# Performance work log

Measured on AMD Instinct MI355X. Metric: run time of the kernel, lower is better.

The kernel has to match this reference:

```python
import jax, jax.numpy as jnp
import numpy as np


def setup_inputs() -> dict:
    key = jax.random.key(0)
    k1, k2 = jax.random.split(key)
    B, A, H, W, C = 4, 9, 256, 256, 9
    F = 64
    lfi = jax.random.normal(k1, (B, A, H, W, C), dtype=jnp.float32)
    f_maps = jax.random.uniform(k2, (B, H, W, F), dtype=jnp.float32)
    return {"lfi": lfi, "f_maps": f_maps}


def reference(lfi, f_maps):
    # height mask: per (b, filter), mean of the [h,w] map over rows, normalized by its max.
    # f_maps: [B, H, W, F] -> hv: [B, W, F]; note original asserts W == H.
    hv = jnp.mean(f_maps, axis=1)                      # [B, W, F]
    hv = hv / jnp.max(hv, axis=1, keepdims=True)       # normalize per (b, f)
    h_mask = jnp.transpose(hv, (0, 2, 1))              # [B, F, H]
    # lfi: [B, A, H, W, C]; h_feat[b,f] = lfi[b] * h_mask[b,f,:] broadcast over H axis,
    # then mean over angular dims A and C -> factorizes as mean(lfi) * h_mask.
    m = jnp.mean(lfi, axis=(1, 4))                     # [B, H, W]
    out = jnp.einsum('bhw,bfh->bhwf', m, h_mask)       # [B, H, W, F]
    return out
```

## Files before the change

### kernel.cpp

```cpp
#include <hip/hip_runtime.h>

#define BB 4
#define AA 9
#define HH 256
#define WW 256
#define CC 9
#define FF 64

__global__ __launch_bounds__(256) void k_stage1(const float* __restrict__ fm,
                                                const float* __restrict__ lfi,
                                                float* __restrict__ hv,
                                                int* __restrict__ maxbuf,
                                                float* __restrict__ m) {
    if (blockIdx.x < BB * WW) {
        const int blk = blockIdx.x;
        const int b = blk >> 8;
        const int w = blk & 255;
        const int f4 = threadIdx.x & 15;
        const int hl = threadIdx.x >> 4;

        const float4* base =
            (const float4*)fm + (((size_t)b * HH) * WW + w) * (FF / 4) + f4;
        float4 acc = make_float4(0.f, 0.f, 0.f, 0.f);
#pragma unroll
        for (int h = hl; h < HH; h += 16) {
            float4 v = base[(size_t)h * WW * (FF / 4)];
            acc.x += v.x; acc.y += v.y; acc.z += v.z; acc.w += v.w;
        }
        __shared__ float sm[16 * FF];
        ((float4*)sm)[hl * 16 + f4] = acc;
        __syncthreads();
        if (threadIdx.x < FF) {
            const int f = threadIdx.x;
            float t = 0.f;
#pragma unroll
            for (int j = 0; j < 16; ++j) t += sm[j * FF + f];
            t *= (1.0f / HH);
            hv[(size_t)blk * FF + f] = t;
            atomicMax(maxbuf + b * FF + f, __float_as_int(t));
        }
    } else {
        const int gid = (blockIdx.x - BB * WW) * 256 + threadIdx.x;
        const int b = gid >> 16;
        const int hw = gid & 65535;

        const size_t astride = (size_t)HH * WW * CC;
        const float* base = lfi + (size_t)b * AA * astride + (size_t)hw * CC;

        float s = 0.f;
#pragma unroll
        for (int a = 0; a < AA; ++a) {
            const float* p = base + (size_t)a * astride;
#pragma unroll
            for (int c = 0; c < CC; ++c) s += p[c];
        }
        m[gid] = s * (1.0f / (AA * CC));
    }
}

__global__ __launch_bounds__(256) void k_out(const float* __restrict__ m,
                                             const float* __restrict__ hv,
                                             const int* __restrict__ maxbuf,
                                             float4* __restrict__ out) {
    const int idx = blockIdx.x * 256 + threadIdx.x;
    const int f4 = idx & 15;
    const int rest = idx >> 4;
    const int h = (rest >> 8) & 255;
    const int b = rest >> 16;

    const float mv = m[rest];
    const float4 hv4 = ((const float4*)hv)[((size_t)(b * HH + h)) * (FF / 4) + f4];
    const int4 mx4 = ((const int4*)maxbuf)[b * (FF / 4) + f4];

    float4 o;
    o.x = mv * hv4.x / __int_as_float(mx4.x);
    o.y = mv * hv4.y / __int_as_float(mx4.y);
    o.z = mv * hv4.z / __int_as_float(mx4.z);
    o.w = mv * hv4.w / __int_as_float(mx4.w);
    out[idx] = o;
}

extern "C" void kernel_launch(void* const* d_in, const int* in_sizes, int n_in,
                              void* d_out, int out_size, void* d_ws, size_t ws_size,
                              hipStream_t stream) {
    const float* lfi = (const float*)d_in[0];
    const float* fm  = (const float*)d_in[1];
    float* out = (float*)d_out;

    char* ws = (char*)d_ws;
    float* hv  = (float*)ws;
    int*   mxb = (int*)(ws + (size_t)BB * WW * FF * 4);
    float* m   = (float*)(ws + (size_t)BB * WW * FF * 4 + 1024);

    hipMemsetAsync(mxb, 0, BB * FF * sizeof(int), stream);
    k_stage1<<<BB * WW + (BB * HH * WW) / 256, 256, 0, stream>>>(fm, lfi, hv, mxb, m);
    k_out<<<(BB * HH * WW * FF / 4) / 256, 256, 0, stream>>>(m, hv, mxb, (float4*)out);
}
```

Before: 47.83 us.

## Restructure f_maps column reduction into row-chunk partials plus separate reduce kernel

The f_maps mean over H is now computed by blocks that each stream a contiguous chunk of full rows, using coalesced float4 loads and 16 accumulators per thread. Each block writes a partial-sum plane, and a new reduce kernel sums the partials, writes hv and does a per-block max before the atomicMax. This replaces the old per-(b,w) strided column walk. The lfi mean path now stages each angular slice through LDS with coalesced float4 loads instead of strided per-thread scalar reads. The cost is an extra kernel launch and partial-buffer traffic, and the chunk count is chosen from the workspace size.

```diff
diff --git a/kernel.cpp b/kernel.cpp
--- a/kernel.cpp
+++ b/kernel.cpp
@@ -6,55 +6,94 @@
 #define WW 256
 #define CC 9
 #define FF 64
+#define WF (WW * FF)
+#define WF4 (WF / 4)
 
-__global__ __launch_bounds__(256) void k_stage1(const float* __restrict__ fm,
-                                                const float* __restrict__ lfi,
-                                                float* __restrict__ hv,
-                                                int* __restrict__ maxbuf,
-                                                float* __restrict__ m) {
-    if (blockIdx.x < BB * WW) {
-        const int blk = blockIdx.x;
-        const int b = blk >> 8;
-        const int w = blk & 255;
-        const int f4 = threadIdx.x & 15;
-        const int hl = threadIdx.x >> 4;
+template <int NCH>
+__global__ __launch_bounds__(256, 2) void k_stage1(const float* __restrict__ fm,
+                                                   const float* __restrict__ lfi,
+                                                   float* __restrict__ partial,
+                                                   float* __restrict__ m) {
+    constexpr int R = HH / NCH;
+    const int t = threadIdx.x;
 
-        const float4* base =
-            (const float4*)fm + (((size_t)b * HH) * WW + w) * (FF / 4) + f4;
-        float4 acc = make_float4(0.f, 0.f, 0.f, 0.f);
+    if (blockIdx.x < BB * NCH) {
+        const int b = blockIdx.x / NCH;
+        const int ch = blockIdx.x % NCH;
+        const float4* row = (const float4*)fm + (size_t)(b * HH + ch * R) * WF4;
+
+        float4 acc[16];
 #pragma unroll
-        for (int h = hl; h < HH; h += 16) {
-            float4 v = base[(size_t)h * WW * (FF / 4)];
-            acc.x += v.x; acc.y += v.y; acc.z += v.z; acc.w += v.w;
+        for (int k = 0; k < 16; ++k) acc[k] = make_float4(0.f, 0.f, 0.f, 0.f);
+
+        for (int r = 0; r < R; ++r) {
+#pragma unroll
+            for (int k = 0; k < 16; ++k) {
+                float4 v = row[(size_t)r * WF4 + k * 256 + t];
+                acc[k].x += v.x; acc[k].y += v.y; acc[k].z += v.z; acc[k].w += v.w;
+            }
         }
-        __shared__ float sm[16 * FF];
-        ((float4*)sm)[hl * 16 + f4] = acc;
-        __syncthreads();
-        if (threadIdx.x < FF) {
-            const int f = threadIdx.x;
-            float t = 0.f;
+        float4* pout = (float4*)partial + (size_t)(b * NCH + ch) * WF4;
 #pragma unroll
-            for (int j = 0; j < 16; ++j) t += sm[j * FF + f];
-            t *= (1.0f / HH);
-            hv[(size_t)blk * FF + f] = t;
-            atomicMax(maxbuf + b * FF + f, __float_as_int(t));
-        }
+        for (int k = 0; k < 16; ++k) pout[k * 256 + t] = acc[k];
     } else {
-        const int gid = (blockIdx.x - BB * WW) * 256 + threadIdx.x;
-        const int b = gid >> 16;
-        const int hw = gid & 65535;
+        const int blkm = blockIdx.x - BB * NCH;
+        const int b = blkm >> 8;
+        const int hw0 = (blkm & 255) * 256;
 
+        __shared__ float lds[256 * CC];
         const size_t astride = (size_t)HH * WW * CC;
-        const float* base = lfi + (size_t)b * AA * astride + (size_t)hw * CC;
+        const float* base = lfi + (size_t)b * AA * astride + (size_t)hw0 * CC;
 
         float s = 0.f;
+        for (int a = 0; a < AA; ++a) {
+            const float4* src = (const float4*)(base + (size_t)a * astride);
+            float4* l4 = (float4*)lds;
+            l4[t] = src[t];
+            l4[t + 256] = src[t + 256];
+            if (t < 64) l4[t + 512] = src[t + 512];
+            __syncthreads();
+            float ps = 0.f;
 #pragma unroll
-        for (int a = 0; a < AA; ++a) {
-            const float* p = base + (size_t)a * astride;
+            for (int c = 0; c < CC; ++c) ps += lds[t * CC + c];
+            s += ps;
+            __syncthreads();
+        }
+        m[(size_t)blkm * 256 + t] = s * (1.0f / (AA * CC));
+    }
+}
+
+template <int NCH>
+__global__ __launch_bounds__(256) void k_reduce(const float* __restrict__ partial,
+                                                float* __restrict__ hv,
+                                                int* __restrict__ maxbuf) {
+    const int t = threadIdx.x;
+    const int b = blockIdx.x >> 4;
+    const int i = blockIdx.x & 15;
+    const int wf4 = i * 256 + t;
+
+    const float4* p4 = (const float4*)partial + (size_t)b * NCH * WF4 + wf4;
+    float4 s = make_float4(0.f, 0.f, 0.f, 0.f);
 #pragma unroll
-            for (int c = 0; c < CC; ++c) s += p[c];
-        }
-        m[gid] = s * (1.0f / (AA * CC));
+    for (int ch = 0; ch < NCH; ++ch) {
+        float4 v = p4[(size_t)ch * WF4];
+        s.x += v.x; s.y += v.y; s.z += v.z; s.w += v.w;
+    }
+    s.x *= (1.0f / HH); s.y *= (1.0f / HH); s.z *= (1.0f / HH); s.w *= (1.0f / HH);
+    ((float4*)hv)[(size_t)b * WF4 + wf4] = s;
+
+    __shared__ float lmax[16][FF];
+    const int wl = t >> 4, f4 = t & 15;
+    lmax[wl][f4 * 4 + 0] = s.x;
+    lmax[wl][f4 * 4 + 1] = s.y;
+    lmax[wl][f4 * 4 + 2] = s.z;
+    lmax[wl][f4 * 4 + 3] = s.w;
+    __syncthreads();
+    if (t < FF) {
+        float mx = lmax[0][t];
+#pragma unroll
+        for (int j = 1; j < 16; ++j) mx = fmaxf(mx, lmax[j][t]);
+        atomicMax(maxbuf + b * FF + t, __float_as_int(mx));
     }
 }
 
@@ -69,7 +108,7 @@
     const int b = rest >> 16;
 
     const float mv = m[rest];
-    const float4 hv4 = ((const float4*)hv)[((size_t)(b * HH + h)) * (FF / 4) + f4];
+    const float4 hv4 = ((const float4*)hv)[(size_t)(b * HH + h) * (FF / 4) + f4];
     const int4 mx4 = ((const int4*)maxbuf)[b * (FF / 4) + f4];
 
     float4 o;
@@ -80,19 +119,38 @@
     out[idx] = o;
 }
 
+template <int NCH>
+static void run_pipeline(const float* lfi, const float* fm, float* out,
+                         char* ws, hipStream_t stream) {
+    float* hv = (float*)ws;
+    int* mxb = (int*)(ws + (size_t)BB * WW * FF * 4);
+    float* m = (float*)(ws + (size_t)BB * WW * FF * 4 + 4096);
+    float* partial = (float*)(ws + (size_t)BB * WW * FF * 4 + 4096 +
+                              (size_t)BB * HH * WW * 4);
+
+    hipMemsetAsync(mxb, 0, BB * FF * sizeof(int), stream);
+    k_stage1<NCH><<<BB * NCH + 1024, 256, 0, stream>>>(fm, lfi, partial, m);
+    k_reduce<NCH><<<BB * 16, 256, 0, stream>>>(partial, hv, mxb);
+    k_out<<<(BB * HH * WW * FF / 4) / 256, 256, 0, stream>>>(m, hv, mxb,
+                                                             (float4*)out);
+}
+
 extern "C" void kernel_launch(void* const* d_in, const int* in_sizes, int n_in,
                               void* d_out, int out_size, void* d_ws, size_t ws_size,
                               hipStream_t stream) {
     const float* lfi = (const float*)d_in[0];
     const float* fm  = (const float*)d_in[1];
     float* out = (float*)d_out;
+    char* ws = (char*)d_ws;
 
-    char* ws = (char*)d_ws;
-    float* hv  = (float*)ws;
-    int*   mxb = (int*)(ws + (size_t)BB * WW * FF * 4);
-    float* m   = (float*)(ws + (size_t)BB * WW * FF * 4 + 1024);
+    const size_t head = (size_t)BB * WW * FF * 4 + 4096 + (size_t)BB * HH * WW * 4;
+    const size_t plane = (size_t)BB * WF * 4;
 
-    hipMemsetAsync(mxb, 0, BB * FF * sizeof(int), stream);
-    k_stage1<<<BB * WW + (BB * HH * WW) / 256, 256, 0, stream>>>(fm, lfi, hv, mxb, m);
-    k_out<<<(BB * HH * WW * FF / 4) / 256, 256, 0, stream>>>(m, hv, mxb, (float4*)out);
+    if (ws_size >= head + 64 * plane) {
+        run_pipeline<64>(lfi, fm, out, ws, stream);
+    } else if (ws_size >= head + 32 * plane) {
+        run_pipeline<32>(lfi, fm, out, ws, stream);
+    } else {
+        run_pipeline<16>(lfi, fm, out, ws, stream);
+    }
 }
```

New measurement: 55.69 us. +16.4%, slower.

## Split height reduction into partial sums and vectorize lfi angular reduction

Applied to the files above, without the earlier changes.

The column-mean reduction over f_maps now runs as a separate kernel. Each block sums a slice of rows for 16 columns into partial buffers, and a second pass combines the partials, writes hv and does a block-local max before one atomicMax per filter. The lfi mean now has each thread handle four pixels with float4 loads, with the angular dimension split across two roles whose partial sums k_out adds together. The output kernel replaces the division with a hardware reciprocal. This adds an extra kernel launch and workspace traffic, and the reciprocal may differ slightly from exact division.

```diff
diff --git a/kernel.cpp b/kernel.cpp
--- a/kernel.cpp
+++ b/kernel.cpp
@@ -6,61 +6,93 @@
 #define WW 256
 #define CC 9
 #define FF 64
+#define WF (WW * FF)
+#define WF4 (WF / 4)
+#define NHQ 8
+#define HQR (HH / NHQ)
 
-__global__ __launch_bounds__(256) void k_stage1(const float* __restrict__ fm,
-                                                const float* __restrict__ lfi,
-                                                float* __restrict__ hv,
-                                                int* __restrict__ maxbuf,
-                                                float* __restrict__ m) {
-    if (blockIdx.x < BB * WW) {
-        const int blk = blockIdx.x;
-        const int b = blk >> 8;
-        const int w = blk & 255;
-        const int f4 = threadIdx.x & 15;
-        const int hl = threadIdx.x >> 4;
+__global__ __launch_bounds__(256) void k_hv(const float* __restrict__ fm,
+                                            float* __restrict__ partial) {
+    const int t = threadIdx.x;
+    const int wc = blockIdx.x & 15;
+    const int hq = (blockIdx.x >> 4) & (NHQ - 1);
+    const int b = blockIdx.x >> 7;
+
+    const float* base = fm + ((size_t)(b * HH + hq * HQR) * WW + wc * 16) * FF +
+                        (t >> 4) * FF + (t & 15) * 4;
+    float4 acc = make_float4(0.f, 0.f, 0.f, 0.f);
+#pragma unroll 8
+    for (int h = 0; h < HQR; ++h) {
+        float4 v = *(const float4*)(base + (size_t)h * WW * FF);
+        acc.x += v.x; acc.y += v.y; acc.z += v.z; acc.w += v.w;
+    }
+    ((float4*)partial)[(size_t)(b * NHQ + hq) * WF4 + wc * 256 + t] = acc;
+}
+
+__global__ __launch_bounds__(256) void k_mred(const float* __restrict__ lfi,
+                                              const float* __restrict__ partial,
+                                              float* __restrict__ mpart,
+                                              float* __restrict__ hv,
+                                              int* __restrict__ mxb) {
+    const int t = threadIdx.x;
+    if (blockIdx.x < 512) {
+        const int role = blockIdx.x >> 8;
+        const int hw4 = (blockIdx.x & 255) * 256 + t;
+        const int b = hw4 >> 14;
+        const int hwl = (hw4 & 16383) * 4;
+        const size_t astride = (size_t)HH * WW * CC;
+        const int a0 = role ? 5 : 0;
+        const int a1 = role ? 9 : 5;
 
         const float4* base =
-            (const float4*)fm + (((size_t)b * HH) * WW + w) * (FF / 4) + f4;
+            (const float4*)(lfi + (size_t)b * AA * astride + (size_t)hwl * CC);
         float4 acc = make_float4(0.f, 0.f, 0.f, 0.f);
+        for (int a = a0; a < a1; ++a) {
+            const float4* p = base + (size_t)a * (astride / 4);
+            float4 v0 = p[0], v1 = p[1], v2 = p[2], v3 = p[3], v4 = p[4];
+            float4 v5 = p[5], v6 = p[6], v7 = p[7], v8 = p[8];
+            acc.x += v0.x + v0.y + v0.z + v0.w + v1.x + v1.y + v1.z + v1.w + v2.x;
+            acc.y += v2.y + v2.z + v2.w + v3.x + v3.y + v3.z + v3.w + v4.x + v4.y;
+            acc.z += v4.z + v4.w + v5.x + v5.y + v5.z + v5.w + v6.x + v6.y + v6.z;
+            acc.w += v6.w + v7.x + v7.y + v7.z + v7.w + v8.x + v8.y + v8.z + v8.w;
+        }
+        ((float4*)mpart)[(size_t)role * 65536 + hw4] = acc;
+    } else {
+        const int rb = blockIdx.x - 512;
+        const int b = rb >> 4;
+        const int i = rb & 15;
+        const int wf4 = i * 256 + t;
+
+        const float4* p4 = (const float4*)partial + (size_t)b * NHQ * WF4 + wf4;
+        float4 s = make_float4(0.f, 0.f, 0.f, 0.f);
 #pragma unroll
-        for (int h = hl; h < HH; h += 16) {
-            float4 v = base[(size_t)h * WW * (FF / 4)];
-            acc.x += v.x; acc.y += v.y; acc.z += v.z; acc.w += v.w;
+        for (int hq = 0; hq < NHQ; ++hq) {
+            float4 v = p4[(size_t)hq * WF4];
+            s.x += v.x; s.y += v.y; s.z += v.z; s.w += v.w;
         }
-        __shared__ float sm[16 * FF];
-        ((float4*)sm)[hl * 16 + f4] = acc;
+        s.x *= (1.0f / HH); s.y *= (1.0f / HH);
+        s.z *= (1.0f / HH); s.w *= (1.0f / HH);
+        ((float4*)hv)[(size_t)b * WF4 + wf4] = s;
+
+        __shared__ float lmax[16][FF];
+        const int wl = t >> 4, f4 = t & 15;
+        lmax[wl][f4 * 4 + 0] = s.x;
+        lmax[wl][f4 * 4 + 1] = s.y;
+        lmax[wl][f4 * 4 + 2] = s.z;
+        lmax[wl][f4 * 4 + 3] = s.w;
         __syncthreads();
-        if (threadIdx.x < FF) {
-            const int f = threadIdx.x;
-            float t = 0.f;
+        if (t < FF) {
+            float mx = lmax[0][t];
 #pragma unroll
-            for (int j = 0; j < 16; ++j) t += sm[j * FF + f];
-            t *= (1.0f / HH);
-            hv[(size_t)blk * FF + f] = t;
-            atomicMax(maxbuf + b * FF + f, __float_as_int(t));
+            for (int j = 1; j < 16; ++j) mx = fmaxf(mx, lmax[j][t]);
+            atomicMax(mxb + b * FF + t, __float_as_int(mx));
         }
-    } else {
-        const int gid = (blockIdx.x - BB * WW) * 256 + threadIdx.x;
-        const int b = gid >> 16;
-        const int hw = gid & 65535;
-
-        const size_t astride = (size_t)HH * WW * CC;
-        const float* base = lfi + (size_t)b * AA * astride + (size_t)hw * CC;
-
-        float s = 0.f;
-#pragma unroll
-        for (int a = 0; a < AA; ++a) {
-            const float* p = base + (size_t)a * astride;
-#pragma unroll
-            for (int c = 0; c < CC; ++c) s += p[c];
-        }
-        m[gid] = s * (1.0f / (AA * CC));
     }
 }
 
-__global__ __launch_bounds__(256) void k_out(const float* __restrict__ m,
+__global__ __launch_bounds__(256) void k_out(const float* __restrict__ mpart,
                                              const float* __restrict__ hv,
-                                             const int* __restrict__ maxbuf,
+                                             const int* __restrict__ mxb,
                                              float4* __restrict__ out) {
     const int idx = blockIdx.x * 256 + threadIdx.x;
     const int f4 = idx & 15;
@@ -68,15 +100,16 @@
     const int h = (rest >> 8) & 255;
     const int b = rest >> 16;
 
-    const float mv = m[rest];
-    const float4 hv4 = ((const float4*)hv)[((size_t)(b * HH + h)) * (FF / 4) + f4];
-    const int4 mx4 = ((const int4*)maxbuf)[b * (FF / 4) + f4];
+    const float mv =
+        (mpart[rest] + mpart[262144 + rest]) * (1.0f / (AA * CC));
+    const float4 hv4 = ((const float4*)hv)[(size_t)(b * HH + h) * (FF / 4) + f4];
+    const int4 mx4 = ((const int4*)mxb)[b * (FF / 4) + f4];
 
     float4 o;
-    o.x = mv * hv4.x / __int_as_float(mx4.x);
-    o.y = mv * hv4.y / __int_as_float(mx4.y);
-    o.z = mv * hv4.z / __int_as_float(mx4.z);
-    o.w = mv * hv4.w / __int_as_float(mx4.w);
+    o.x = mv * hv4.x * __builtin_amdgcn_rcpf(__int_as_float(mx4.x));
+    o.y = mv * hv4.y * __builtin_amdgcn_rcpf(__int_as_float(mx4.y));
+    o.z = mv * hv4.z * __builtin_amdgcn_rcpf(__int_as_float(mx4.z));
+    o.w = mv * hv4.w * __builtin_amdgcn_rcpf(__int_as_float(mx4.w));
     out[idx] = o;
 }
 
@@ -86,13 +119,16 @@
     const float* lfi = (const float*)d_in[0];
     const float* fm  = (const float*)d_in[1];
     float* out = (float*)d_out;
+    char* ws = (char*)d_ws;
 
-    char* ws = (char*)d_ws;
-    float* hv  = (float*)ws;
-    int*   mxb = (int*)(ws + (size_t)BB * WW * FF * 4);
-    float* m   = (float*)(ws + (size_t)BB * WW * FF * 4 + 1024);
+    float* hv = (float*)ws;
+    int* mxb = (int*)(ws + 262144);
+    float* mpart = (float*)(ws + 262144 + 4096);
+    float* partial = (float*)(ws + 262144 + 4096 + 2097152);
 
     hipMemsetAsync(mxb, 0, BB * FF * sizeof(int), stream);
-    k_stage1<<<BB * WW + (BB * HH * WW) / 256, 256, 0, stream>>>(fm, lfi, hv, mxb, m);
-    k_out<<<(BB * HH * WW * FF / 4) / 256, 256, 0, stream>>>(m, hv, mxb, (float4*)out);
+    k_hv<<<BB * NHQ * 16, 256, 0, stream>>>(fm, partial);
+    k_mred<<<512 + BB * 16, 256, 0, stream>>>(lfi, partial, mpart, hv, mxb);
+    k_out<<<(BB * HH * WW * FF / 4) / 256, 256, 0, stream>>>(mpart, hv, mxb,
+                                                             (float4*)out);
 }
```

New measurement: 49.44 us. 3.4% more time.

## Fuse lfi angular mean into output kernel and split hv reduction kernel

Applied to the files above, without the earlier changes.

Moves the lfi mean computation out of the first kernel and into the output kernel. Each block computes m for one (b,h) row into LDS and then writes all 64 filter outputs for that row, so the m intermediate no longer goes to global memory. The hv reduction now uses a two-level shared-memory tree and issues four atomics per thread. Division is replaced by a hardware reciprocal applied once per thread. The trade-off is less overlap between the lfi reads and the f_maps reduction, plus slightly lower precision from the approximate reciprocal.

```diff
diff --git a/kernel.cpp b/kernel.cpp
--- a/kernel.cpp
+++ b/kernel.cpp
@@ -7,77 +7,97 @@
 #define CC 9
 #define FF 64
 
-__global__ __launch_bounds__(256) void k_stage1(const float* __restrict__ fm,
-                                                const float* __restrict__ lfi,
-                                                float* __restrict__ hv,
-                                                int* __restrict__ maxbuf,
-                                                float* __restrict__ m) {
-    if (blockIdx.x < BB * WW) {
-        const int blk = blockIdx.x;
-        const int b = blk >> 8;
-        const int w = blk & 255;
-        const int f4 = threadIdx.x & 15;
-        const int hl = threadIdx.x >> 4;
+__global__ __launch_bounds__(256) void k_hv(const float* __restrict__ fm,
+                                            float* __restrict__ hv,
+                                            int* __restrict__ mxb) {
+    const int t = threadIdx.x;
+    const int w = blockIdx.x & 255;
+    const int b = blockIdx.x >> 8;
+    const int f4 = t & 15;
+    const int hl = t >> 4;
 
-        const float4* base =
-            (const float4*)fm + (((size_t)b * HH) * WW + w) * (FF / 4) + f4;
-        float4 acc = make_float4(0.f, 0.f, 0.f, 0.f);
+    const float4* base = (const float4*)fm +
+                         ((size_t)(b * HH + hl) * WW + w) * (FF / 4) + f4;
+    const size_t hstep = (size_t)16 * WW * (FF / 4);
+    float4 acc = make_float4(0.f, 0.f, 0.f, 0.f);
 #pragma unroll
-        for (int h = hl; h < HH; h += 16) {
-            float4 v = base[(size_t)h * WW * (FF / 4)];
-            acc.x += v.x; acc.y += v.y; acc.z += v.z; acc.w += v.w;
-        }
-        __shared__ float sm[16 * FF];
-        ((float4*)sm)[hl * 16 + f4] = acc;
-        __syncthreads();
-        if (threadIdx.x < FF) {
-            const int f = threadIdx.x;
-            float t = 0.f;
-#pragma unroll
-            for (int j = 0; j < 16; ++j) t += sm[j * FF + f];
-            t *= (1.0f / HH);
-            hv[(size_t)blk * FF + f] = t;
-            atomicMax(maxbuf + b * FF + f, __float_as_int(t));
-        }
-    } else {
-        const int gid = (blockIdx.x - BB * WW) * 256 + threadIdx.x;
-        const int b = gid >> 16;
-        const int hw = gid & 65535;
+    for (int i = 0; i < 16; ++i) {
+        float4 v = base[i * hstep];
+        acc.x += v.x; acc.y += v.y; acc.z += v.z; acc.w += v.w;
+    }
 
-        const size_t astride = (size_t)HH * WW * CC;
-        const float* base = lfi + (size_t)b * AA * astride + (size_t)hw * CC;
-
-        float s = 0.f;
-#pragma unroll
-        for (int a = 0; a < AA; ++a) {
-            const float* p = base + (size_t)a * astride;
-#pragma unroll
-            for (int c = 0; c < CC; ++c) s += p[c];
-        }
-        m[gid] = s * (1.0f / (AA * CC));
+    __shared__ float4 sm[16][16];
+    __shared__ float4 sm2[4][16];
+    sm[hl][f4] = acc;
+    __syncthreads();
+    if (t < 64) {
+        const int q = t >> 4, f = t & 15;
+        float4 s0 = sm[q * 4 + 0][f], s1 = sm[q * 4 + 1][f];
+        float4 s2 = sm[q * 4 + 2][f], s3 = sm[q * 4 + 3][f];
+        float4 r;
+        r.x = (s0.x + s1.x) + (s2.x + s3.x);
+        r.y = (s0.y + s1.y) + (s2.y + s3.y);
+        r.z = (s0.z + s1.z) + (s2.z + s3.z);
+        r.w = (s0.w + s1.w) + (s2.w + s3.w);
+        sm2[q][f] = r;
+    }
+    __syncthreads();
+    if (t < 16) {
+        float4 s0 = sm2[0][t], s1 = sm2[1][t], s2 = sm2[2][t], s3 = sm2[3][t];
+        float4 r;
+        r.x = ((s0.x + s1.x) + (s2.x + s3.x)) * (1.0f / HH);
+        r.y = ((s0.y + s1.y) + (s2.y + s3.y)) * (1.0f / HH);
+        r.z = ((s0.z + s1.z) + (s2.z + s3.z)) * (1.0f / HH);
+        r.w = ((s0.w + s1.w) + (s2.w + s3.w)) * (1.0f / HH);
+        ((float4*)hv)[(size_t)(b * WW + w) * (FF / 4) + t] = r;
+        int* mp = mxb + b * FF + t * 4;
+        atomicMax(mp + 0, __float_as_int(r.x));
+        atomicMax(mp + 1, __float_as_int(r.y));
+        atomicMax(mp + 2, __float_as_int(r.z));
+        atomicMax(mp + 3, __float_as_int(r.w));
     }
 }
 
-__global__ __launch_bounds__(256) void k_out(const float* __restrict__ m,
-                                             const float* __restrict__ hv,
-                                             const int* __restrict__ maxbuf,
-                                             float4* __restrict__ out) {
-    const int idx = blockIdx.x * 256 + threadIdx.x;
-    const int f4 = idx & 15;
-    const int rest = idx >> 4;
-    const int h = (rest >> 8) & 255;
-    const int b = rest >> 16;
+__global__ __launch_bounds__(256) void k_mout(const float* __restrict__ lfi,
+                                              const float* __restrict__ hv,
+                                              const int* __restrict__ mxb,
+                                              float4* __restrict__ out) {
+    const int t = threadIdx.x;
+    const int bh = blockIdx.x;
+    const int b = bh >> 8;
+    const int h = bh & 255;
+    const int f4 = t & 15;
 
-    const float mv = m[rest];
-    const float4 hv4 = ((const float4*)hv)[((size_t)(b * HH + h)) * (FF / 4) + f4];
-    const int4 mx4 = ((const int4*)maxbuf)[b * (FF / 4) + f4];
+    const float4 hv4 = ((const float4*)hv)[(size_t)bh * (FF / 4) + f4];
+    const int4 mx4 = ((const int4*)mxb)[b * (FF / 4) + f4];
+    float4 hvn;
+    hvn.x = hv4.x * __builtin_amdgcn_rcpf(__int_as_float(mx4.x));
+    hvn.y = hv4.y * __builtin_amdgcn_rcpf(__int_as_float(mx4.y));
+    hvn.z = hv4.z * __builtin_amdgcn_rcpf(__int_as_float(mx4.z));
+    hvn.w = hv4.w * __builtin_amdgcn_rcpf(__int_as_float(mx4.w));
 
-    float4 o;
-    o.x = mv * hv4.x / __int_as_float(mx4.x);
-    o.y = mv * hv4.y / __int_as_float(mx4.y);
-    o.z = mv * hv4.z / __int_as_float(mx4.z);
-    o.w = mv * hv4.w / __int_as_float(mx4.w);
-    out[idx] = o;
+    const size_t astride = (size_t)HH * WW * CC;
+    const float* base = lfi + (size_t)b * AA * astride +
+                        ((size_t)h * WW + t) * CC;
+    float s = 0.f;
+#pragma unroll
+    for (int a = 0; a < AA; ++a) {
+        const float* p = base + (size_t)a * astride;
+#pragma unroll
+        for (int c = 0; c < CC; ++c) s += p[c];
+    }
+    __shared__ float m_lds[WW];
+    m_lds[t] = s * (1.0f / (AA * CC));
+    __syncthreads();
+
+    float4* ob = out + (size_t)bh * (WW * FF / 4);
+#pragma unroll
+    for (int k = 0; k < 16; ++k) {
+        const float mv = m_lds[k * 16 + (t >> 4)];
+        float4 o;
+        o.x = mv * hvn.x; o.y = mv * hvn.y; o.z = mv * hvn.z; o.w = mv * hvn.w;
+        ob[k * 256 + t] = o;
+    }
 }
 
 extern "C" void kernel_launch(void* const* d_in, const int* in_sizes, int n_in,
@@ -86,13 +106,12 @@
     const float* lfi = (const float*)d_in[0];
     const float* fm  = (const float*)d_in[1];
     float* out = (float*)d_out;
+    char* ws = (char*)d_ws;
 
-    char* ws = (char*)d_ws;
-    float* hv  = (float*)ws;
-    int*   mxb = (int*)(ws + (size_t)BB * WW * FF * 4);
-    float* m   = (float*)(ws + (size_t)BB * WW * FF * 4 + 1024);
+    float* hv = (float*)ws;
+    int* mxb = (int*)(ws + (size_t)BB * WW * FF * 4);
 
     hipMemsetAsync(mxb, 0, BB * FF * sizeof(int), stream);
-    k_stage1<<<BB * WW + (BB * HH * WW) / 256, 256, 0, stream>>>(fm, lfi, hv, mxb, m);
-    k_out<<<(BB * HH * WW * FF / 4) / 256, 256, 0, stream>>>(m, hv, mxb, (float4*)out);
+    k_hv<<<BB * WW, 256, 0, stream>>>(fm, hv, mxb);
+    k_mout<<<BB * HH, 256, 0, stream>>>(lfi, hv, mxb, (float4*)out);
 }
```

Result: slower. 69.40 us (+45.1%).
